# Kernel optimization log

Measured on AMD Instinct MI355X. Metric: run time of the kernel, lower is better.

The kernel has to match this reference:

```python
import jax, jax.numpy as jnp
import numpy as np
import math

D = 4096            # input dim and all hidden dims
TOKENS = (4, 2048)  # batch, seq
P = 0.8             # excitatory fraction for EI layers


def conn_dense(kernel, x):
    # bool kernel interpreted as +1 (True) / -1 (False)
    w = jnp.where(kernel, jnp.asarray(1.0, x.dtype), jnp.asarray(-1.0, x.dtype))
    return x @ w


def ei_dense(x, kernel, scale, p):
    in_dim = x.shape[-1]
    ne = round(in_dim * p)  # excitatory count
    x_exc = x[..., :ne]
    x_inh = x[..., ne:]
    xx = jnp.concatenate([x_exc, (-p / (1.0 - p)) * x_inh], axis=-1)
    return scale * conn_dense(kernel, xx)


def setup_inputs() -> dict:
    key = jax.random.key(0)
    ks = jax.random.split(key, 4)
    x = jax.random.normal(ks[0], (*TOKENS, D), dtype=jnp.float32)
    k0 = jax.random.bernoulli(ks[1], 0.5, (D, D))
    k1 = jax.random.bernoulli(ks[2], 0.5, (D, D))
    k2 = jax.random.bernoulli(ks[3], 0.5, (D, D))
    s = jnp.asarray(1.0 / math.sqrt(D), dtype=jnp.float32)
    return {"x": x, "k0": k0, "s0": s, "k1": k1, "s1": s, "k2": k2, "s2": s}


def reference(x, k0, s0, k1, s1, k2, s2):
    # layer 0: Dense_01 (plain +/-1 matmul, scale), then relu*2
    h = s0 * conn_dense(k0, x)
    h = jax.nn.relu(h) * 2.0
    # layer 1: Dense_EI, then relu*2
    h = ei_dense(h, k1, s1, P)
    h = jax.nn.relu(h) * 2.0
    # layer 2: Dense_EI (no activation on last layer)
    return ei_dense(h, k2, s2, P)
```

## Files before the change

### kernel.cpp

```cpp
#include <hip/hip_runtime.h>
#include <stdint.h>

#define DD 4096
#define NE_IDX 3277

typedef __attribute__((ext_vector_type(8))) short short8;
typedef __attribute__((ext_vector_type(4))) float f32x4;
typedef __attribute__((ext_vector_type(4))) unsigned int u32x4;

__device__ __forceinline__ unsigned short f2bf(float f) {
    unsigned int u = __float_as_uint(f);
    u += 0x7fffu + ((u >> 16) & 1u);
    return (unsigned short)(u >> 16);
}

__device__ __forceinline__ void gload16(const void* g, void* l) {
    __builtin_amdgcn_global_load_lds(
        (const __attribute__((address_space(1))) unsigned int*)g,
        (__attribute__((address_space(3))) unsigned int*)l,
        16, 0, 0);
}

__global__ void detect_kernel(const unsigned int* __restrict__ k0, int* __restrict__ flag) {
    if (blockIdx.x == 0 && threadIdx.x == 0) {
        int ok4 = 1;
        for (int i = 0; i < 256; ++i) {
            unsigned int v = k0[i];
            if (!(v == 0u || v == 1u || v == 0x3f800000u)) { ok4 = 0; break; }
        }
        *flag = ok4;
    }
}

__global__ void pack_x_kernel(const float* __restrict__ x, unsigned short* __restrict__ xb, int n8) {
    const int stride = gridDim.x * blockDim.x;
    for (int i = blockIdx.x * blockDim.x + threadIdx.x; i < n8; i += stride) {
        const float4* p = (const float4*)(x + (size_t)i * 8);
        float4 a = p[0], b = p[1];
        short8 r;
        r[0] = (short)f2bf(a.x); r[1] = (short)f2bf(a.y);
        r[2] = (short)f2bf(a.z); r[3] = (short)f2bf(a.w);
        r[4] = (short)f2bf(b.x); r[5] = (short)f2bf(b.y);
        r[6] = (short)f2bf(b.z); r[7] = (short)f2bf(b.w);
        *(short8*)(xb + (size_t)i * 8) = r;
    }
}

__global__ void pack_w_kernel(const void* __restrict__ kin, unsigned short* __restrict__ wt,
                              const float* __restrict__ sptr, float inh, int ne,
                              const int* __restrict__ flag) {
    __shared__ unsigned short tile[64][68];
    const int elem4 = *flag;
    const float s = *sptr;
    const int i0 = blockIdx.x * 64;
    const int j0 = blockIdx.y * 64;
    const int t = threadIdx.x;
    {
        const int il = t >> 2;
        const int jc = (t & 3) * 16;
        const int gi = i0 + il;
        const float mag = s * ((gi < ne) ? 1.0f : inh);
        const unsigned short pos = f2bf(mag);
        const unsigned short neg = f2bf(-mag);
        if (elem4) {
            const unsigned int* k32 = (const unsigned int*)kin + (size_t)gi * DD + j0 + jc;
            #pragma unroll
            for (int q = 0; q < 4; ++q) {
                u32x4 v = *(const u32x4*)(k32 + q * 4);
                #pragma unroll
                for (int e = 0; e < 4; ++e)
                    tile[il][jc + q * 4 + e] = v[e] ? pos : neg;
            }
        } else {
            const unsigned char* k8 = (const unsigned char*)kin + (size_t)gi * DD + j0 + jc;
            u32x4 v = *(const u32x4*)k8;
            #pragma unroll
            for (int q = 0; q < 4; ++q) {
                unsigned int w = v[q];
                tile[il][jc + q * 4 + 0] = (w & 0xffu) ? pos : neg;
                tile[il][jc + q * 4 + 1] = ((w >> 8) & 0xffu) ? pos : neg;
                tile[il][jc + q * 4 + 2] = ((w >> 16) & 0xffu) ? pos : neg;
                tile[il][jc + q * 4 + 3] = ((w >> 24) & 0xffu) ? pos : neg;
            }
        }
    }
    __syncthreads();
    {
        const int jl = t >> 2;
        const int ic = (t & 3) * 16;
        short8 o0, o1;
        #pragma unroll
        for (int e = 0; e < 8; ++e) o0[e] = (short)tile[ic + e][jl];
        #pragma unroll
        for (int e = 0; e < 8; ++e) o1[e] = (short)tile[ic + 8 + e][jl];
        unsigned short* dst = wt + (size_t)(j0 + jl) * DD + i0 + ic;
        *(short8*)(dst) = o0;
        *(short8*)(dst + 8) = o1;
    }
}

#define PHASE(MH, NH, LA, LB, STAGE_STMT, EB) do {                              \
    if (LA) {                                                                   \
        _Pragma("unroll")                                                       \
        for (int m = 0; m < 4; ++m) {                                           \
            af[0][m] = *(const short8*)(Lc + (ab[(MH)*4+m] ^ kx0));             \
            af[1][m] = *(const short8*)(Lc + (ab[(MH)*4+m] ^ kx1));             \
        }                                                                       \
    }                                                                           \
    if (LB) {                                                                   \
        _Pragma("unroll")                                                       \
        for (int n = 0; n < 2; ++n) {                                           \
            bf[0][n] = *(const short8*)(Lc + (bb[(NH)*2+n] ^ kx0));             \
            bf[1][n] = *(const short8*)(Lc + (bb[(NH)*2+n] ^ kx1));             \
        }                                                                       \
    }                                                                           \
    STAGE_STMT;                                                                 \
    asm volatile("s_waitcnt vmcnt(4)" ::: "memory");                            \
    __builtin_amdgcn_s_barrier();                                               \
    asm volatile("s_waitcnt lgkmcnt(0)" ::: "memory");                          \
    __builtin_amdgcn_sched_barrier(0);                                          \
    __builtin_amdgcn_s_setprio(1);                                              \
    _Pragma("unroll")                                                           \
    for (int kk = 0; kk < 2; ++kk)                                              \
        _Pragma("unroll")                                                       \
        for (int m = 0; m < 4; ++m)                                             \
            _Pragma("unroll")                                                   \
            for (int n = 0; n < 2; ++n)                                         \
                acc[(MH)*4+m][(NH)*2+n] = __builtin_amdgcn_mfma_f32_16x16x32_bf16( \
                    af[kk][m], bf[kk][n], acc[(MH)*4+m][(NH)*2+n], 0, 0, 0);    \
    __builtin_amdgcn_s_setprio(0);                                              \
    __builtin_amdgcn_sched_barrier(0);                                          \
    if (EB) __builtin_amdgcn_s_barrier();                                       \
} while (0)

template <int MODE>
__global__ __launch_bounds__(512, 2)
void gemm256_kernel(const unsigned short* __restrict__ A,
                    const unsigned short* __restrict__ Bt,
                    void* __restrict__ Cout)
{
    __shared__ unsigned short L[65536];
    const char* Lc = (const char*)L;

    const int tid  = threadIdx.x;
    const int lane = tid & 63;
    const int fr   = lane & 15;
    const int fg   = lane >> 4;
    const int wave = tid >> 6;
    const int wr   = wave >> 2;
    const int wc   = wave & 3;

    int wg = blockIdx.x;
    const int per = gridDim.x >> 3;
    wg = (wg & 7) * per + (wg >> 3);
    const int tm = wg >> 4;
    const int tn = wg & 15;

    const size_t arow0 = (size_t)tm * 256;
    const size_t brow0 = (size_t)tn * 256;

    const int rq = tid >> 3;
    const int wq = (tid >> 6) << 3;
    const int srcoff = (((tid & 7) ^ ((tid >> 3) & 7)) << 3);

    auto stageA = [&](int sb, int c, int kt) {
        #pragma unroll
        for (int q = 0; q < 2; ++q) {
            const int dr = c * 64 + q * 128 + rq;
            gload16(A + ((arow0 + dr) << 12) + kt + srcoff,
                    (void*)&L[sb + ((c * 64 + q * 128 + wq) << 6)]);
        }
    };
    auto stageB = [&](int sb, int c, int kt) {
        #pragma unroll
        for (int q = 0; q < 2; ++q) {
            const int lr  = q * 64 + rq;
            const int dr  = c * 32 + (lr & 31) + (lr >> 5) * 64;
            const int wlr = q * 64 + wq;
            const int wdr = c * 32 + (wlr & 31) + (wlr >> 5) * 64;
            gload16(Bt + ((brow0 + dr) << 12) + kt + srcoff,
                    (void*)&L[sb + 16384 + (wdr << 6)]);
        }
    };

    const int kx0 = fg << 4;
    const int kx1 = (4 + fg) << 4;
    int ab[8], bb[4];
    #pragma unroll
    for (int m = 0; m < 8; ++m) {
        const int r = wr * 128 + m * 16 + fr;
        ab[m] = r * 128 + ((r & 7) << 4);
    }
    #pragma unroll
    for (int n = 0; n < 4; ++n) {
        const int r = wc * 64 + n * 16 + fr;
        bb[n] = 32768 + r * 128 + ((r & 7) << 4);
    }

    short8 af[2][4], bf[2][2];
    f32x4 acc[8][4];
    #pragma unroll
    for (int m = 0; m < 8; ++m)
        #pragma unroll
        for (int n = 0; n < 4; ++n)
            acc[m][n] = (f32x4){0.f, 0.f, 0.f, 0.f};

    stageA(0, 0, 0); stageB(0, 0, 0); stageB(0, 1, 0); stageA(0, 1, 0);
    asm volatile("s_waitcnt vmcnt(4)" ::: "memory");
    __builtin_amdgcn_s_barrier();
    __builtin_amdgcn_sched_barrier(0);

    for (int t = 0; t < 63; ++t) {
        const int sb  = ((t & 1) ^ 1) * 32768;
        const int kt1 = (t + 1) * 64;
        PHASE(0, 0, 1, 1, stageA(sb, 0, kt1), 0);
        PHASE(0, 1, 0, 1, stageB(sb, 0, kt1), 0);
        PHASE(1, 1, 1, 0, stageB(sb, 1, kt1), 0);
        PHASE(1, 0, 0, 1, stageA(sb, 1, kt1), 1);
        #pragma unroll
        for (int i = 0; i < 8; ++i) ab[i] ^= 65536;
        #pragma unroll
        for (int i = 0; i < 4; ++i) bb[i] ^= 65536;
    }
    asm volatile("s_waitcnt vmcnt(0)" ::: "memory");
    __builtin_amdgcn_s_barrier();
    __builtin_amdgcn_sched_barrier(0);
    PHASE(0, 0, 1, 1, (void)0, 0);
    PHASE(0, 1, 0, 1, (void)0, 0);
    PHASE(1, 1, 1, 0, (void)0, 0);
    PHASE(1, 0, 0, 1, (void)0, 0);

    const int orow0 = tm * 256 + wr * 128;
    const int ocol0 = tn * 256 + wc * 64;
    #pragma unroll
    for (int m = 0; m < 8; ++m) {
        #pragma unroll
        for (int n = 0; n < 4; ++n) {
            #pragma unroll
            for (int j = 0; j < 4; ++j) {
                const int row = orow0 + m * 16 + fg * 4 + j;
                const int col = ocol0 + n * 16 + fr;
                float v = acc[m][n][j];
                if (MODE == 1) {
                    v = fmaxf(v, 0.0f) * 2.0f;
                    ((unsigned short*)Cout)[((size_t)row << 12) + col] = f2bf(v);
                } else {
                    ((float*)Cout)[((size_t)row << 12) + col] = v;
                }
            }
        }
    }
}

extern "C" void kernel_launch(void* const* d_in, const int* in_sizes, int n_in,
                              void* d_out, int out_size, void* d_ws, size_t ws_size,
                              hipStream_t stream) {
    const float* x  = (const float*)d_in[0];
    const void*  k0 = d_in[1];
    const float* s0 = (const float*)d_in[2];
    const void*  k1 = d_in[3];
    const float* s1 = (const float*)d_in[4];
    const void*  k2 = d_in[5];
    const float* s2 = (const float*)d_in[6];

    const int M = in_sizes[0] / DD;

    const size_t act_bytes = (size_t)M * DD * 2;
    const size_t w_bytes   = (size_t)DD * DD * 2;
    const size_t need      = act_bytes * 2 + w_bytes + 256;
    if (ws_size < need) return;

    char* ws = (char*)d_ws;
    unsigned short* xb = (unsigned short*)ws;
    unsigned short* h1 = (unsigned short*)(ws + act_bytes);
    unsigned short* wt = (unsigned short*)(ws + act_bytes * 2);
    int* flag          = (int*)(ws + act_bytes * 2 + w_bytes);

    detect_kernel<<<1, 64, 0, stream>>>((const unsigned int*)k0, flag);
    pack_x_kernel<<<2048, 256, 0, stream>>>(x, xb, M * DD / 8);

    dim3 pw_grid(DD / 64, DD / 64);
    const int gemm_grid = (M / 256) * (DD / 256);

    pack_w_kernel<<<pw_grid, 256, 0, stream>>>(k0, wt, s0, 1.0f, DD, flag);
    gemm256_kernel<1><<<gemm_grid, 512, 0, stream>>>(xb, wt, h1);

    pack_w_kernel<<<pw_grid, 256, 0, stream>>>(k1, wt, s1, -4.0f, NE_IDX, flag);
    gemm256_kernel<1><<<gemm_grid, 512, 0, stream>>>(h1, wt, xb);

    pack_w_kernel<<<pw_grid, 256, 0, stream>>>(k2, wt, s2, -4.0f, NE_IDX, flag);
    gemm256_kernel<0><<<gemm_grid, 512, 0, stream>>>(xb, wt, (float*)d_out);
}
```

Measured before the change: 711.1 us.

## Switch GEMM inner loop from 16x16x32 to 32x32x16 bf16 MFMA tiles

Replaces the 16x16x32 MFMA microkernel with 32x32x16 bf16 MFMA, rebuilding the LDS fragment addressing, the swizzle indexing and the accumulator layout (4x2 f32x16 instead of 8x4 f32x4). Larger MFMA tiles cut the number of LDS fragment reads per FLOP and the instruction count per phase. The epilogue store indexing is rewritten to match the 32x32 output layout. This risks LDS bank conflicts with the new swizzle and a different register pressure profile.

```diff
diff --git a/kernel.cpp b/kernel.cpp
--- a/kernel.cpp
+++ b/kernel.cpp
@@ -6,6 +6,7 @@
 
 typedef __attribute__((ext_vector_type(8))) short short8;
 typedef __attribute__((ext_vector_type(4))) float f32x4;
+typedef __attribute__((ext_vector_type(16))) float f32x16;
 typedef __attribute__((ext_vector_type(4))) unsigned int u32x4;
 
 __device__ __forceinline__ unsigned short f2bf(float f) {
@@ -99,20 +100,18 @@
     }
 }
 
-#define PHASE(MH, NH, LA, LB, STAGE_STMT, EB) do {                              \
+#define PH32(MH, NH, LA, LB, STAGE_STMT, EB) do {                               \
     if (LA) {                                                                   \
         _Pragma("unroll")                                                       \
-        for (int m = 0; m < 4; ++m) {                                           \
-            af[0][m] = *(const short8*)(Lc + (ab[(MH)*4+m] ^ kx0));             \
-            af[1][m] = *(const short8*)(Lc + (ab[(MH)*4+m] ^ kx1));             \
-        }                                                                       \
+        for (int mi = 0; mi < 2; ++mi)                                          \
+            _Pragma("unroll")                                                   \
+            for (int s = 0; s < 4; ++s)                                         \
+                af[mi][s] = *(const short8*)(Lc + (abh[(MH)*2+mi] ^ (s<<5)));   \
     }                                                                           \
     if (LB) {                                                                   \
         _Pragma("unroll")                                                       \
-        for (int n = 0; n < 2; ++n) {                                           \
-            bf[0][n] = *(const short8*)(Lc + (bb[(NH)*2+n] ^ kx0));             \
-            bf[1][n] = *(const short8*)(Lc + (bb[(NH)*2+n] ^ kx1));             \
-        }                                                                       \
+        for (int s = 0; s < 4; ++s)                                             \
+            bf[s] = *(const short8*)(Lc + (bbh[(NH)] ^ (s<<5)));                \
     }                                                                           \
     STAGE_STMT;                                                                 \
     asm volatile("s_waitcnt vmcnt(4)" ::: "memory");                            \
@@ -121,13 +120,11 @@
     __builtin_amdgcn_sched_barrier(0);                                          \
     __builtin_amdgcn_s_setprio(1);                                              \
     _Pragma("unroll")                                                           \
-    for (int kk = 0; kk < 2; ++kk)                                              \
+    for (int s = 0; s < 4; ++s)                                                 \
         _Pragma("unroll")                                                       \
-        for (int m = 0; m < 4; ++m)                                             \
-            _Pragma("unroll")                                                   \
-            for (int n = 0; n < 2; ++n)                                         \
-                acc[(MH)*4+m][(NH)*2+n] = __builtin_amdgcn_mfma_f32_16x16x32_bf16( \
-                    af[kk][m], bf[kk][n], acc[(MH)*4+m][(NH)*2+n], 0, 0, 0);    \
+        for (int mi = 0; mi < 2; ++mi)                                          \
+            acc[(MH)*2+mi][(NH)] = __builtin_amdgcn_mfma_f32_32x32x16_bf16(     \
+                af[mi][s], bf[s], acc[(MH)*2+mi][(NH)], 0, 0, 0);               \
     __builtin_amdgcn_s_setprio(0);                                              \
     __builtin_amdgcn_sched_barrier(0);                                          \
     if (EB) __builtin_amdgcn_s_barrier();                                       \
@@ -144,8 +141,8 @@
 
     const int tid  = threadIdx.x;
     const int lane = tid & 63;
-    const int fr   = lane & 15;
-    const int fg   = lane >> 4;
+    const int l31  = lane & 31;
+    const int hb   = lane >> 5;
     const int wave = tid >> 6;
     const int wr   = wave >> 2;
     const int wc   = wave & 3;
@@ -183,27 +180,27 @@
         }
     };
 
-    const int kx0 = fg << 4;
-    const int kx1 = (4 + fg) << 4;
-    int ab[8], bb[4];
-    #pragma unroll
-    for (int m = 0; m < 8; ++m) {
-        const int r = wr * 128 + m * 16 + fr;
-        ab[m] = r * 128 + ((r & 7) << 4);
-    }
-    #pragma unroll
-    for (int n = 0; n < 4; ++n) {
-        const int r = wc * 64 + n * 16 + fr;
-        bb[n] = 32768 + r * 128 + ((r & 7) << 4);
-    }
-
-    short8 af[2][4], bf[2][2];
-    f32x4 acc[8][4];
-    #pragma unroll
-    for (int m = 0; m < 8; ++m)
-        #pragma unroll
-        for (int n = 0; n < 4; ++n)
-            acc[m][n] = (f32x4){0.f, 0.f, 0.f, 0.f};
+    int abh[4], bbh[2];
+    #pragma unroll
+    for (int mt = 0; mt < 4; ++mt) {
+        const int r = wr * 128 + mt * 32 + l31;
+        abh[mt] = r * 128 + ((hb ^ (r & 7)) << 4);
+    }
+    #pragma unroll
+    for (int nt = 0; nt < 2; ++nt) {
+        const int r = wc * 64 + nt * 32 + l31;
+        bbh[nt] = 32768 + r * 128 + ((hb ^ (r & 7)) << 4);
+    }
+
+    short8 af[2][4], bf[4];
+    f32x16 acc[4][2];
+    #pragma unroll
+    for (int m = 0; m < 4; ++m)
+        #pragma unroll
+        for (int n = 0; n < 2; ++n)
+            #pragma unroll
+            for (int e = 0; e < 16; ++e)
+                acc[m][n][e] = 0.f;
 
     stageA(0, 0, 0); stageB(0, 0, 0); stageB(0, 1, 0); stageA(0, 1, 0);
     asm volatile("s_waitcnt vmcnt(4)" ::: "memory");
@@ -213,34 +210,33 @@
     for (int t = 0; t < 63; ++t) {
         const int sb  = ((t & 1) ^ 1) * 32768;
         const int kt1 = (t + 1) * 64;
-        PHASE(0, 0, 1, 1, stageA(sb, 0, kt1), 0);
-        PHASE(0, 1, 0, 1, stageB(sb, 0, kt1), 0);
-        PHASE(1, 1, 1, 0, stageB(sb, 1, kt1), 0);
-        PHASE(1, 0, 0, 1, stageA(sb, 1, kt1), 1);
-        #pragma unroll
-        for (int i = 0; i < 8; ++i) ab[i] ^= 65536;
-        #pragma unroll
-        for (int i = 0; i < 4; ++i) bb[i] ^= 65536;
+        PH32(0, 0, 1, 1, stageA(sb, 0, kt1), 0);
+        PH32(0, 1, 0, 1, stageB(sb, 0, kt1), 0);
+        PH32(1, 1, 1, 0, stageB(sb, 1, kt1), 0);
+        PH32(1, 0, 0, 1, stageA(sb, 1, kt1), 1);
+        #pragma unroll
+        for (int i = 0; i < 4; ++i) abh[i] ^= 65536;
+        bbh[0] ^= 65536; bbh[1] ^= 65536;
     }
     asm volatile("s_waitcnt vmcnt(0)" ::: "memory");
     __builtin_amdgcn_s_barrier();
     __builtin_amdgcn_sched_barrier(0);
-    PHASE(0, 0, 1, 1, (void)0, 0);
-    PHASE(0, 1, 0, 1, (void)0, 0);
-    PHASE(1, 1, 1, 0, (void)0, 0);
-    PHASE(1, 0, 0, 1, (void)0, 0);
-
-    const int orow0 = tm * 256 + wr * 128;
-    const int ocol0 = tn * 256 + wc * 64;
-    #pragma unroll
-    for (int m = 0; m < 8; ++m) {
-        #pragma unroll
-        for (int n = 0; n < 4; ++n) {
-            #pragma unroll
-            for (int j = 0; j < 4; ++j) {
-                const int row = orow0 + m * 16 + fg * 4 + j;
-                const int col = ocol0 + n * 16 + fr;
-                float v = acc[m][n][j];
+    PH32(0, 0, 1, 1, (void)0, 0);
+    PH32(0, 1, 0, 1, (void)0, 0);
+    PH32(1, 1, 1, 0, (void)0, 0);
+    PH32(1, 0, 0, 1, (void)0, 0);
+
+    const int orow0 = tm * 256 + wr * 128 + hb * 4;
+    const int ocol0 = tn * 256 + wc * 64 + l31;
+    #pragma unroll
+    for (int mt = 0; mt < 4; ++mt) {
+        #pragma unroll
+        for (int nt = 0; nt < 2; ++nt) {
+            #pragma unroll
+            for (int reg = 0; reg < 16; ++reg) {
+                const int row = orow0 + mt * 32 + (reg & 3) + 8 * (reg >> 2);
+                const int col = ocol0 + nt * 32;
+                float v = acc[mt][nt][reg];
                 if (MODE == 1) {
                     v = fmaxf(v, 0.0f) * 2.0f;
                     ((unsigned short*)Cout)[((size_t)row << 12) + col] = f2bf(v);
```

After: 766.2 us. +7.8%, slower.

## Deepen GEMM prefetch by staging half-tiles into the other buffer earlier

Applied to the files above, without the earlier changes.

Restructures the double-buffered main loop so that half-tiles for the next k-step are loaded as soon as their buffer region is consumed. It unrolls two k-steps per iteration and adds extra prologue stages and a specialized epilogue. The vmcnt wait moves to the end of selected phases and each phase now always ends with a barrier. The aim is to hide more global-load latency, at the cost of more barriers and more complex correctness conditions on buffer reuse.

```diff
diff --git a/kernel.cpp b/kernel.cpp
--- a/kernel.cpp
+++ b/kernel.cpp
@@ -20,6 +20,8 @@
         (__attribute__((address_space(3))) unsigned int*)l,
         16, 0, 0);
 }
+
+#define BAR  __builtin_amdgcn_s_barrier()
 
 __global__ void detect_kernel(const unsigned int* __restrict__ k0, int* __restrict__ flag) {
     if (blockIdx.x == 0 && threadIdx.x == 0) {
@@ -99,7 +101,7 @@
     }
 }
 
-#define PHASE(MH, NH, LA, LB, STAGE_STMT, EB) do {                              \
+#define PHASE(MH, NH, LA, LB, STAGE_STMT, VM) do {                              \
     if (LA) {                                                                   \
         _Pragma("unroll")                                                       \
         for (int m = 0; m < 4; ++m) {                                           \
@@ -110,12 +112,11 @@
     if (LB) {                                                                   \
         _Pragma("unroll")                                                       \
         for (int n = 0; n < 2; ++n) {                                           \
-            bf[0][n] = *(const short8*)(Lc + (bb[(NH)*2+n] ^ kx0));             \
-            bf[1][n] = *(const short8*)(Lc + (bb[(NH)*2+n] ^ kx1));             \
+            bfr[0][n] = *(const short8*)(Lc + (bb[(NH)*2+n] ^ kx0));            \
+            bfr[1][n] = *(const short8*)(Lc + (bb[(NH)*2+n] ^ kx1));            \
         }                                                                       \
     }                                                                           \
     STAGE_STMT;                                                                 \
-    asm volatile("s_waitcnt vmcnt(4)" ::: "memory");                            \
     __builtin_amdgcn_s_barrier();                                               \
     asm volatile("s_waitcnt lgkmcnt(0)" ::: "memory");                          \
     __builtin_amdgcn_sched_barrier(0);                                          \
@@ -127,10 +128,12 @@
             _Pragma("unroll")                                                   \
             for (int n = 0; n < 2; ++n)                                         \
                 acc[(MH)*4+m][(NH)*2+n] = __builtin_amdgcn_mfma_f32_16x16x32_bf16( \
-                    af[kk][m], bf[kk][n], acc[(MH)*4+m][(NH)*2+n], 0, 0, 0);    \
+                    af[kk][m], bfr[kk][n], acc[(MH)*4+m][(NH)*2+n], 0, 0, 0);   \
     __builtin_amdgcn_s_setprio(0);                                              \
     __builtin_amdgcn_sched_barrier(0);                                          \
-    if (EB) __builtin_amdgcn_s_barrier();                                       \
+    if ((VM) == 1) asm volatile("s_waitcnt vmcnt(4)" ::: "memory");             \
+    if ((VM) == 2) asm volatile("s_waitcnt vmcnt(0)" ::: "memory");             \
+    __builtin_amdgcn_s_barrier();                                               \
 } while (0)
 
 template <int MODE>
@@ -197,7 +200,7 @@
         bb[n] = 32768 + r * 128 + ((r & 7) << 4);
     }
 
-    short8 af[2][4], bf[2][2];
+    short8 af[2][4], bfr[2][2];
     f32x4 acc[8][4];
     #pragma unroll
     for (int m = 0; m < 8; ++m)
@@ -205,30 +208,48 @@
         for (int n = 0; n < 4; ++n)
             acc[m][n] = (f32x4){0.f, 0.f, 0.f, 0.f};
 
-    stageA(0, 0, 0); stageB(0, 0, 0); stageB(0, 1, 0); stageA(0, 1, 0);
+    stageA(0, 0, 0); stageA(0, 1, 0); stageB(0, 0, 0); stageB(0, 1, 0);
+    stageA(32768, 0, 64); stageB(32768, 1, 64);
     asm volatile("s_waitcnt vmcnt(4)" ::: "memory");
-    __builtin_amdgcn_s_barrier();
+    BAR;
     __builtin_amdgcn_sched_barrier(0);
 
-    for (int t = 0; t < 63; ++t) {
-        const int sb  = ((t & 1) ^ 1) * 32768;
-        const int kt1 = (t + 1) * 64;
-        PHASE(0, 0, 1, 1, stageA(sb, 0, kt1), 0);
-        PHASE(0, 1, 0, 1, stageB(sb, 0, kt1), 0);
-        PHASE(1, 1, 1, 0, stageB(sb, 1, kt1), 0);
-        PHASE(1, 0, 0, 1, stageA(sb, 1, kt1), 1);
+    for (int t = 0; t < 31; ++t) {
+        const int kt1 = (2 * t + 1) * 64;
+        const int kt2 = (2 * t + 2) * 64;
+        const int kt3 = (2 * t + 3) * 64;
+        PHASE(0, 0, 1, 1, stageA(32768, 1, kt1), 0);
+        PHASE(0, 1, 0, 1, stageB(32768, 0, kt1), 0);
+        PHASE(1, 1, 1, 0, stageA(0, 0, kt2), 0);
+        PHASE(1, 0, 0, 1, stageB(0, 1, kt2), 1);
         #pragma unroll
         for (int i = 0; i < 8; ++i) ab[i] ^= 65536;
         #pragma unroll
         for (int i = 0; i < 4; ++i) bb[i] ^= 65536;
-    }
-    asm volatile("s_waitcnt vmcnt(0)" ::: "memory");
-    __builtin_amdgcn_s_barrier();
-    __builtin_amdgcn_sched_barrier(0);
-    PHASE(0, 0, 1, 1, (void)0, 0);
-    PHASE(0, 1, 0, 1, (void)0, 0);
-    PHASE(1, 1, 1, 0, (void)0, 0);
-    PHASE(1, 0, 0, 1, (void)0, 0);
+        PHASE(0, 0, 1, 1, stageB(0, 0, kt2), 0);
+        PHASE(0, 1, 0, 1, stageA(0, 1, kt2), 0);
+        PHASE(1, 1, 1, 0, stageA(32768, 0, kt3), 0);
+        PHASE(1, 0, 0, 1, stageB(32768, 1, kt3), 1);
+        #pragma unroll
+        for (int i = 0; i < 8; ++i) ab[i] ^= 65536;
+        #pragma unroll
+        for (int i = 0; i < 4; ++i) bb[i] ^= 65536;
+    }
+    {
+        const int kt1 = 63 * 64;
+        PHASE(0, 0, 1, 1, stageA(32768, 1, kt1), 0);
+        PHASE(0, 1, 0, 1, stageB(32768, 0, kt1), 0);
+        PHASE(1, 1, 1, 0, (void)0, 0);
+        PHASE(1, 0, 0, 1, (void)0, 2);
+        #pragma unroll
+        for (int i = 0; i < 8; ++i) ab[i] ^= 65536;
+        #pragma unroll
+        for (int i = 0; i < 4; ++i) bb[i] ^= 65536;
+        PHASE(0, 0, 1, 1, (void)0, 0);
+        PHASE(0, 1, 0, 1, (void)0, 0);
+        PHASE(1, 1, 1, 0, (void)0, 0);
+        PHASE(1, 0, 0, 1, (void)0, 0);
+    }
 
     const int orow0 = tm * 256 + wr * 128;
     const int ocol0 = tn * 256 + wc * 64;
```

After: 743.3 us. +4.5%, slower.
